# Optimization experiments

Measured on AMD Instinct MI355X. Metric: run time of the kernel, lower is better.

## Reference

```python
import jax, jax.numpy as jnp
import numpy as np

COMMITMENT_COST = 0.25


def l2norm(x, eps=1e-12):
    # F.normalize along last dim
    n = jnp.linalg.norm(x, axis=-1, keepdims=True)
    return x / jnp.maximum(n, eps)


def vector_quantize(x, codebook, commitment_cost):
    """Euclidean VQ: cdist + argmin, straight-through, VQ loss + perplexity.
    x: (B, N, D), codebook: (K, D)."""
    B, N, D = x.shape
    K = codebook.shape[0]
    flat = x.reshape(-1, D)  # (BN, D)
    # squared euclidean distances via expansion (no (BN,K,D) intermediate)
    d = (jnp.sum(flat * flat, axis=-1, keepdims=True)
         - 2.0 * flat @ codebook.T
         + jnp.sum(codebook * codebook, axis=-1))  # (BN, K)
    idx = jnp.argmin(d, axis=-1)  # (BN,)
    q = codebook[idx]  # (BN, D)
    # VQ losses
    e_latent = jnp.mean((jax.lax.stop_gradient(q) - flat) ** 2)
    q_latent = jnp.mean((q - jax.lax.stop_gradient(flat)) ** 2)
    loss = q_latent + commitment_cost * e_latent
    # perplexity over codebook usage (bincount, not dense one-hot)
    counts = jnp.zeros((K,), flat.dtype).at[idx].add(1.0)
    probs = counts / idx.shape[0]
    perplexity = jnp.exp(-jnp.sum(probs * jnp.log(probs + 1e-10)))
    return idx.reshape(B, N), perplexity, loss


def transform_mfcc(X):
    # wave_embedding.transform_freq: normalize frames, then rfft -> real -> bins 2:40
    Xn = l2norm(X)
    spec = jnp.fft.rfft(Xn, axis=-1).real[..., 2:40]  # (B, N, 38)
    return l2norm(spec)  # mfcc_embedding.norm_fn


def setup_inputs() -> dict:
    key = jax.random.key(0)
    k1, k2, k3 = jax.random.split(key, 3)
    X = jax.random.normal(k1, (16, 4096, 80), dtype=jnp.float32)
    wave_codebook = jax.random.normal(k2, (1024, 80), dtype=jnp.float32)
    mfcc_codebook = jax.random.normal(k3, (256, 38), dtype=jnp.float32)
    return {"X": X, "wave_codebook": wave_codebook, "mfcc_codebook": mfcc_codebook}


def reference(X, wave_codebook, mfcc_codebook):
    K_wave = wave_codebook.shape[0]
    wave_idx, wave_ppl, wave_loss = vector_quantize(X, wave_codebook, COMMITMENT_COST)
    X_mfcc = transform_mfcc(X)
    mfcc_idx, mfcc_ppl, mfcc_loss = vector_quantize(X_mfcc, mfcc_codebook, COMMITMENT_COST)
    mfcc_idx = mfcc_idx + K_wave
    # rearrange stack([wave, mfcc], dim=1): 'b c n -> b (n c)' -> interleave per frame
    B, N = wave_idx.shape
    encodings = jnp.stack([wave_idx, mfcc_idx], axis=-1).reshape(B, 2 * N)
    return encodings, wave_ppl, wave_loss, mfcc_ppl, mfcc_loss
```

## Files before the change

### kernel.cpp

```cpp
#include <hip/hip_runtime.h>
#include <hip/hip_bf16.h>
#include <math.h>


#define NROWS 65536
#define DW    80
#define KW    1024
#define DM    38
#define KM    256

typedef __attribute__((ext_vector_type(8))) short bf16x8;
typedef __attribute__((ext_vector_type(4))) float f32x4;

__device__ __forceinline__ void bf16split(float v, short& h, short& l) {
    __hip_bfloat16 hb = __float2bfloat16(v);
    float hf = __bfloat162float(hb);
    __hip_bfloat16 lb = __float2bfloat16(v - hf);
    h = *(short*)&hb;
    l = *(short*)&lb;
}

__device__ __forceinline__ void bf16split3(float v, short& a, short& b, short& c) {
    __hip_bfloat16 h = __float2bfloat16(v);
    float hf = __bfloat162float(h);
    float r = v - hf;
    __hip_bfloat16 m = __float2bfloat16(r);
    float mf = __bfloat162float(m);
    __hip_bfloat16 lo = __float2bfloat16(r - mf);
    a = *(short*)&h; b = *(short*)&m; c = *(short*)&lo;
}

__device__ __forceinline__ bf16x8 bf8zero() {
    bf16x8 z;
    #pragma unroll
    for (int j = 0; j < 8; ++j) z[j] = 0;
    return z;
}

__device__ __forceinline__ void wvq_tile(
    const bf16x8 (&Ah)[4][3], const bf16x8 (&Al)[4][3],
    const bf16x8 (&bh)[3], const bf16x8 (&bl)[3],
    float cnv, int idx0, float (&bd)[4][4], int (&bi)[4][4])
{
    f32x4 aL[4], aH[4];
    #pragma unroll
    for (int rt = 0; rt < 4; ++rt) {
        aL[rt] = (f32x4){0.f, 0.f, 0.f, 0.f};
        aH[rt] = (f32x4){0.f, 0.f, 0.f, 0.f};
    }
    #pragma unroll
    for (int s = 0; s < 3; ++s) {
        #pragma unroll
        for (int rt = 0; rt < 4; ++rt)
            aL[rt] = __builtin_amdgcn_mfma_f32_16x16x32_bf16(Al[rt][s], bl[s], aL[rt], 0, 0, 0);
        #pragma unroll
        for (int rt = 0; rt < 4; ++rt)
            aL[rt] = __builtin_amdgcn_mfma_f32_16x16x32_bf16(Ah[rt][s], bl[s], aL[rt], 0, 0, 0);
        #pragma unroll
        for (int rt = 0; rt < 4; ++rt)
            aH[rt] = __builtin_amdgcn_mfma_f32_16x16x32_bf16(Al[rt][s], bh[s], aH[rt], 0, 0, 0);
        #pragma unroll
        for (int rt = 0; rt < 4; ++rt)
            aH[rt] = __builtin_amdgcn_mfma_f32_16x16x32_bf16(Ah[rt][s], bh[s], aH[rt], 0, 0, 0);
    }
    #pragma unroll
    for (int rt = 0; rt < 4; ++rt)
        #pragma unroll
        for (int i = 0; i < 4; ++i) {
            float d = fmaf(-2.f, aL[rt][i] + aH[rt][i], cnv);
            if (d < bd[rt][i]) { bd[rt][i] = d; bi[rt][i] = idx0; }
        }
}

#define WS_SUMS   0
#define WS_HIST   256
#define WS_CNW    5376
#define WS_CNM    9472
#define WS_CTF    10496
#define WS_CBF    33536
#define WS_CWH    107264
#define WS_CWL    303872

__global__ __launch_bounds__(256) void prep_kernel(
    const float* __restrict__ cbw, const float* __restrict__ cbm,
    float* __restrict__ sums, int* __restrict__ hist,
    float* __restrict__ cn_w, float* __restrict__ cn_m,
    short* __restrict__ ctf, short* __restrict__ cbf,
    short* __restrict__ cwh, short* __restrict__ cwl)
{
    int idx = blockIdx.x * 256 + threadIdx.x;
    if (idx < 12288) {
        const int f = idx;
        const int ct = f / 192, rem = f % 192, s = rem >> 6, l = rem & 63;
        const int code = ct * 16 + (l & 15);
        const int k0 = 32 * s + 8 * (l >> 4);
        bf16x8 h, lo;
        if (k0 < DW) {
            const float4* p = (const float4*)(cbw + (size_t)code * DW + k0);
            float4 u = p[0], v = p[1];
            float fv[8] = {u.x, u.y, u.z, u.w, v.x, v.y, v.z, v.w};
            #pragma unroll
            for (int j = 0; j < 8; ++j) {
                short hh, ll;
                bf16split(fv[j], hh, ll);
                h[j] = hh; lo[j] = ll;
            }
        } else { h = bf8zero(); lo = bf8zero(); }
        *(bf16x8*)&cwh[(size_t)f * 8] = h;
        *(bf16x8*)&cwl[(size_t)f * 8] = lo;
    } else if (idx < 16128) {
        int t = idx - 12288;
        int col, k;
        if (t < 3072) {
            int j = t & 7, l = (t >> 3) & 63, tt = t >> 9;
            col = (tt >> 1) * 16 + (l & 15);
            k = 32 * (tt & 1) + 8 * (l >> 4) + j;
        } else {
            int i2 = t - 3072;
            int j = i2 & 7, l = (i2 >> 3) & 31, ct = i2 >> 8;
            col = ct * 16 + (l & 15);
            k = 64 + 8 * (l >> 4) + j;
        }
        float v = (col < DM)
            ? (float)cos(2.0 * 3.14159265358979323846 * (double)((col + 2) * k) / 80.0)
            : 0.f;
        short a, b, c; bf16split3(v, a, b, c);
        ctf[t] = a; ctf[3840 + t] = b; ctf[7680 + t] = c;
    } else if (idx < 28416) {
        int i3 = idx - 16128;
        int code, k;
        if (i3 < 8192) {
            int j = i3 & 7, l = (i3 >> 3) & 63, ct = i3 >> 9;
            code = ct * 16 + (l & 15);
            k = 8 * (l >> 4) + j;
        } else {
            int i4 = i3 - 8192;
            int j = i4 & 7, l = (i4 >> 3) & 31, ct = i4 >> 8;
            code = ct * 16 + (l & 15);
            k = 32 + 8 * (l >> 4) + j;
        }
        float v = (k < DM) ? cbm[(size_t)code * DM + k] : 0.f;
        short a, b, c; bf16split3(v, a, b, c);
        cbf[i3] = a; cbf[12288 + i3] = b; cbf[24576 + i3] = c;
    } else if (idx < 29440) {
        int i = idx - 28416;
        const float* p = cbw + (size_t)i * DW;
        float s = 0.f;
        for (int k = 0; k < DW; ++k) s = fmaf(p[k], p[k], s);
        cn_w[i] = s;
    } else if (idx < 29696) {
        int i = idx - 29440;
        const float* p = cbm + (size_t)i * DM;
        float s = 0.f;
        for (int j = 0; j < DM; ++j) s = fmaf(p[j], p[j], s);
        cn_m[i] = s;
    } else if (idx < 30976) {
        hist[idx - 29696] = 0;
    } else if (idx == 30976) sums[0] = 0.f;
    else if (idx == 30977)   sums[1] = 0.f;
}

__global__ __launch_bounds__(256, 2) void wave_vq_mfma(
    const float* __restrict__ X, const short* __restrict__ cwh,
    const short* __restrict__ cwl, const float* __restrict__ cn,
    float* __restrict__ out, float* __restrict__ sums)
{
    __shared__ float sd[2][64][16];
    __shared__ int   si[2][64][16];
    __shared__ float redw[2];

    const int tid  = threadIdx.x;
    const int l    = tid & 63;
    const int qu   = tid >> 6;
    const int grp  = qu >> 1;
    const int half = qu & 1;
    const int c16  = l & 15;
    const int g    = l >> 4;
    const size_t rowbase = (size_t)blockIdx.x * 128 + (size_t)grp * 64;

    bf16x8 Ah[4][3], Al[4][3];
    float xs2[4] = {0.f, 0.f, 0.f, 0.f};
    #pragma unroll
    for (int rt = 0; rt < 4; ++rt) {
        #pragma unroll
        for (int s = 0; s < 3; ++s) {
            const int k0 = 32 * s + 8 * g;
            bf16x8 ah, al;
            if (k0 < DW) {
                const float4* ap =
                    (const float4*)(X + (rowbase + rt * 16 + c16) * DW + k0);
                float4 u = ap[0], w = ap[1];
                float f[8] = {u.x, u.y, u.z, u.w, w.x, w.y, w.z, w.w};
                #pragma unroll
                for (int j = 0; j < 8; ++j) {
                    short hh, ll;
                    bf16split(f[j], hh, ll);
                    ah[j] = hh; al[j] = ll;
                    xs2[rt] = fmaf(f[j], f[j], xs2[rt]);
                }
            } else {
                ah = bf8zero(); al = bf8zero();
            }
            Ah[rt][s] = ah; Al[rt][s] = al;
        }
    }
    #pragma unroll
    for (int rt = 0; rt < 4; ++rt) {
        xs2[rt] += __shfl_xor(xs2[rt], 16, 64);
        xs2[rt] += __shfl_xor(xs2[rt], 32, 64);
    }

    float bd[4][4];
    int   bi[4][4];
    #pragma unroll
    for (int rt = 0; rt < 4; ++rt)
        #pragma unroll
        for (int i = 0; i < 4; ++i) { bd[rt][i] = 3.4e38f; bi[rt][i] = 0; }

    const bf16x8* Hp = (const bf16x8*)cwh + l;
    const bf16x8* Lp = (const bf16x8*)cwl + l;
    const int ct0 = half * 32;

    bf16x8 b0h[3], b0l[3], b1h[3], b1l[3];
    float cn0, cn1;
    #pragma unroll
    for (int s = 0; s < 3; ++s) {
        b0h[s] = Hp[(ct0 * 3 + s) * 64];
        b0l[s] = Lp[(ct0 * 3 + s) * 64];
    }
    cn0 = cn[ct0 * 16 + c16];

    #pragma unroll 1
    for (int ctl = 0; ctl < 32; ctl += 2) {
        const int ct = ct0 + ctl;
        #pragma unroll
        for (int s = 0; s < 3; ++s) {
            b1h[s] = Hp[((ct + 1) * 3 + s) * 64];
            b1l[s] = Lp[((ct + 1) * 3 + s) * 64];
        }
        cn1 = cn[(ct + 1) * 16 + c16];
        wvq_tile(Ah, Al, b0h, b0l, cn0, ct * 16 + c16, bd, bi);
        if (ctl + 2 < 32) {
            #pragma unroll
            for (int s = 0; s < 3; ++s) {
                b0h[s] = Hp[((ct + 2) * 3 + s) * 64];
                b0l[s] = Lp[((ct + 2) * 3 + s) * 64];
            }
            cn0 = cn[(ct + 2) * 16 + c16];
        }
        wvq_tile(Ah, Al, b1h, b1l, cn1, (ct + 1) * 16 + c16, bd, bi);
    }

    if (half == 1) {
        #pragma unroll
        for (int rt = 0; rt < 4; ++rt)
            #pragma unroll
            for (int i = 0; i < 4; ++i) {
                sd[grp][l][rt * 4 + i] = bd[rt][i];
                si[grp][l][rt * 4 + i] = bi[rt][i];
            }
    }
    __syncthreads();
    if (half == 0) {
        float lw = 0.f;
        #pragma unroll
        for (int rt = 0; rt < 4; ++rt) {
            #pragma unroll
            for (int i = 0; i < 4; ++i) {
                float d = bd[rt][i]; int ix = bi[rt][i];
                float dp = sd[grp][l][rt * 4 + i];
                int   ip = si[grp][l][rt * 4 + i];
                if (dp < d || (dp == d && ip < ix)) { d = dp; ix = ip; }
                #pragma unroll
                for (int m = 1; m < 16; m <<= 1) {
                    float d2 = __shfl_xor(d, m, 64);
                    int   i2 = __shfl_xor(ix, m, 64);
                    if (d2 < d || (d2 == d && i2 < ix)) { d = d2; ix = i2; }
                }
                float xn = __shfl(xs2[rt], (l & 48) + 4 * (l >> 4) + i, 64);
                if (c16 == 0) {
                    size_t row = rowbase + rt * 16 + 4 * g + i;
                    out[2 * row] = (float)ix;
                    lw += d + xn;
                }
            }
        }
        #pragma unroll
        for (int m = 1; m < 64; m <<= 1) lw += __shfl_xor(lw, m, 64);
        if (l == 0) redw[grp] = lw;
    }
    __syncthreads();
    if (tid == 0) atomicAdd(&sums[0], redw[0] + redw[1]);
}

__global__ __launch_bounds__(256, 2) void mfcc_mfma(
    const float* __restrict__ X, const float* __restrict__ cn_m,
    const short* __restrict__ ctf, const short* __restrict__ cbf,
    float* __restrict__ out, float* __restrict__ sums)
{
    __shared__ float XF[2][64 * 49];
    __shared__ float sd[2][64][16];
    __shared__ int   si[2][64][16];
    __shared__ float CN[KM];
    __shared__ float red2[2];

    const int tid  = threadIdx.x;
    const int l    = tid & 63;
    const int qu   = tid >> 6;
    const int grp  = qu >> 1;
    const int half = qu & 1;
    const int c16  = l & 15;
    const int g    = l >> 4;
    const size_t rowbase = (size_t)blockIdx.x * 128 + (size_t)grp * 64;

    CN[tid] = cn_m[tid];

    float* xfl = &XF[grp][0];

    #pragma unroll 1
    for (int rt2 = 0; rt2 < 2; ++rt2) {
        const int rt = half * 2 + rt2;
        bf16x8 A0[3], A1[3], A2[3];
        #pragma unroll
        for (int s = 0; s < 3; ++s) {
            const int k0 = 32 * s + 8 * g;
            if (k0 < DW) {
                const float4* ap =
                    (const float4*)(X + (rowbase + rt * 16 + c16) * DW + k0);
                float4 u = ap[0], v = ap[1];
                float f[8] = {u.x, u.y, u.z, u.w, v.x, v.y, v.z, v.w};
                bf16x8 a0, a1, a2;
                #pragma unroll
                for (int j = 0; j < 8; ++j) {
                    short aa, bb, cc;
                    bf16split3(f[j], aa, bb, cc);
                    a0[j] = aa; a1[j] = bb; a2[j] = cc;
                }
                A0[s] = a0; A1[s] = a1; A2[s] = a2;
            } else {
                A0[s] = bf8zero(); A1[s] = bf8zero(); A2[s] = bf8zero();
            }
        }

        f32x4 accA[3], accB[3];
        #pragma unroll
        for (int ct = 0; ct < 3; ++ct) {
            accA[ct] = (f32x4){0.f, 0.f, 0.f, 0.f};
            accB[ct] = (f32x4){0.f, 0.f, 0.f, 0.f};
        }

        #pragma unroll
        for (int s = 0; s < 3; ++s) {
            #pragma unroll
            for (int ct = 0; ct < 3; ++ct) {
                bf16x8 b0, b1, b2;
                if (s < 2) {
                    const int off = ((ct * 2 + s) * 64 + l) * 8;
                    b0 = *(const bf16x8*)&ctf[off];
                    b1 = *(const bf16x8*)&ctf[3840 + off];
                    b2 = *(const bf16x8*)&ctf[7680 + off];
                } else if (l < 32) {
                    const int off = 3072 + (ct * 32 + l) * 8;
                    b0 = *(const bf16x8*)&ctf[off];
                    b1 = *(const bf16x8*)&ctf[3840 + off];
                    b2 = *(const bf16x8*)&ctf[7680 + off];
                } else {
                    b0 = bf8zero(); b1 = bf8zero(); b2 = bf8zero();
                }
                accA[ct] = __builtin_amdgcn_mfma_f32_16x16x32_bf16(A2[s], b0, accA[ct], 0, 0, 0);
                accA[ct] = __builtin_amdgcn_mfma_f32_16x16x32_bf16(A1[s], b1, accA[ct], 0, 0, 0);
                accA[ct] = __builtin_amdgcn_mfma_f32_16x16x32_bf16(A0[s], b2, accA[ct], 0, 0, 0);
                accB[ct] = __builtin_amdgcn_mfma_f32_16x16x32_bf16(A1[s], b0, accB[ct], 0, 0, 0);
                accB[ct] = __builtin_amdgcn_mfma_f32_16x16x32_bf16(A0[s], b1, accB[ct], 0, 0, 0);
                accB[ct] = __builtin_amdgcn_mfma_f32_16x16x32_bf16(A0[s], b0, accB[ct], 0, 0, 0);
            }
        }

        f32x4 acc[3];
        #pragma unroll
        for (int ct = 0; ct < 3; ++ct) acc[ct] = accA[ct] + accB[ct];

        #pragma unroll
        for (int i = 0; i < 4; ++i) {
            float n2 = acc[0][i] * acc[0][i];
            n2 = fmaf(acc[1][i], acc[1][i], n2);
            n2 = fmaf(acc[2][i], acc[2][i], n2);
            #pragma unroll
            for (int m = 1; m < 16; m <<= 1) n2 += __shfl_xor(n2, m, 64);
            float inv = 1.0f / fmaxf(sqrtf(n2), 1e-12f);
            const int row_l = rt * 16 + 4 * g + i;
            #pragma unroll
            for (int ct = 0; ct < 3; ++ct)
                xfl[row_l * 49 + ct * 16 + c16] = acc[ct][i] * inv;
        }
    }
    __syncthreads();

    bf16x8 X0[4][3], X1[4][3];
    #pragma unroll
    for (int rt = 0; rt < 4; ++rt) {
        const int r0 = rt * 16 + c16;
        {
            const float* p = &xfl[r0 * 49 + 8 * g];
            bf16x8 q0, q1, q2;
            #pragma unroll
            for (int j = 0; j < 8; ++j) {
                short aa, bb, cc;
                bf16split3(p[j], aa, bb, cc);
                q0[j] = aa; q1[j] = bb; q2[j] = cc;
            }
            X0[rt][0] = q0; X0[rt][1] = q1; X0[rt][2] = q2;
        }
        if (g < 2) {
            const float* p = &xfl[r0 * 49 + 32 + 8 * g];
            bf16x8 q0, q1, q2;
            #pragma unroll
            for (int j = 0; j < 8; ++j) {
                short aa, bb, cc;
                bf16split3(p[j], aa, bb, cc);
                q0[j] = aa; q1[j] = bb; q2[j] = cc;
            }
            X1[rt][0] = q0; X1[rt][1] = q1; X1[rt][2] = q2;
        } else {
            X1[rt][0] = bf8zero(); X1[rt][1] = bf8zero(); X1[rt][2] = bf8zero();
        }
    }

    float bd[4][4];
    int   bi[4][4];
    #pragma unroll
    for (int rt = 0; rt < 4; ++rt)
        #pragma unroll
        for (int i = 0; i < 4; ++i) { bd[rt][i] = 3.4e38f; bi[rt][i] = 0; }

    #pragma unroll 1
    for (int ctl = 0; ctl < 8; ++ctl) {
        const int ct = half * 8 + ctl;
        bf16x8 B0[3], B1[3];
        const int off0 = (ct * 64 + l) * 8;
        B0[0] = *(const bf16x8*)&cbf[off0];
        B0[1] = *(const bf16x8*)&cbf[12288 + off0];
        B0[2] = *(const bf16x8*)&cbf[24576 + off0];
        if (l < 32) {
            const int off1 = 8192 + (ct * 32 + l) * 8;
            B1[0] = *(const bf16x8*)&cbf[off1];
            B1[1] = *(const bf16x8*)&cbf[12288 + off1];
            B1[2] = *(const bf16x8*)&cbf[24576 + off1];
        } else {
            B1[0] = bf8zero(); B1[1] = bf8zero(); B1[2] = bf8zero();
        }
        const float cnv = CN[ct * 16 + c16];
        const int idxbase = ct * 16 + c16;
        #pragma unroll
        for (int rt = 0; rt < 4; ++rt) {
            f32x4 p0 = (f32x4){0.f, 0.f, 0.f, 0.f};
            f32x4 q0 = (f32x4){0.f, 0.f, 0.f, 0.f};
            f32x4 p1 = (f32x4){0.f, 0.f, 0.f, 0.f};
            f32x4 q1 = (f32x4){0.f, 0.f, 0.f, 0.f};
            p0 = __builtin_amdgcn_mfma_f32_16x16x32_bf16(X0[rt][2], B0[0], p0, 0, 0, 0);
            p0 = __builtin_amdgcn_mfma_f32_16x16x32_bf16(X0[rt][1], B0[1], p0, 0, 0, 0);
            p0 = __builtin_amdgcn_mfma_f32_16x16x32_bf16(X0[rt][0], B0[2], p0, 0, 0, 0);
            q0 = __builtin_amdgcn_mfma_f32_16x16x32_bf16(X0[rt][1], B0[0], q0, 0, 0, 0);
            q0 = __builtin_amdgcn_mfma_f32_16x16x32_bf16(X0[rt][0], B0[1], q0, 0, 0, 0);
            q0 = __builtin_amdgcn_mfma_f32_16x16x32_bf16(X0[rt][0], B0[0], q0, 0, 0, 0);
            p1 = __builtin_amdgcn_mfma_f32_16x16x32_bf16(X1[rt][2], B1[0], p1, 0, 0, 0);
            p1 = __builtin_amdgcn_mfma_f32_16x16x32_bf16(X1[rt][1], B1[1], p1, 0, 0, 0);
            p1 = __builtin_amdgcn_mfma_f32_16x16x32_bf16(X1[rt][0], B1[2], p1, 0, 0, 0);
            q1 = __builtin_amdgcn_mfma_f32_16x16x32_bf16(X1[rt][1], B1[0], q1, 0, 0, 0);
            q1 = __builtin_amdgcn_mfma_f32_16x16x32_bf16(X1[rt][0], B1[1], q1, 0, 0, 0);
            q1 = __builtin_amdgcn_mfma_f32_16x16x32_bf16(X1[rt][0], B1[0], q1, 0, 0, 0);
            #pragma unroll
            for (int i = 0; i < 4; ++i) {
                float d = fmaf(-2.f, (p0[i] + q0[i]) + (p1[i] + q1[i]), cnv);
                if (d < bd[rt][i]) { bd[rt][i] = d; bi[rt][i] = idxbase; }
            }
        }
    }

    if (half == 1) {
        #pragma unroll
        for (int rt = 0; rt < 4; ++rt)
            #pragma unroll
            for (int i = 0; i < 4; ++i) {
                sd[grp][l][rt * 4 + i] = bd[rt][i];
                si[grp][l][rt * 4 + i] = bi[rt][i];
            }
    }
    __syncthreads();
    if (half == 0) {
        float lm = 0.f;
        #pragma unroll
        for (int rt = 0; rt < 4; ++rt) {
            #pragma unroll
            for (int i = 0; i < 4; ++i) {
                float d = bd[rt][i]; int ix = bi[rt][i];
                float dp = sd[grp][l][rt * 4 + i];
                int   ip = si[grp][l][rt * 4 + i];
                if (dp < d || (dp == d && ip < ix)) { d = dp; ix = ip; }
                #pragma unroll
                for (int m = 1; m < 16; m <<= 1) {
                    float d2 = __shfl_xor(d, m, 64);
                    int   i2 = __shfl_xor(ix, m, 64);
                    if (d2 < d || (d2 == d && i2 < ix)) { d = d2; ix = i2; }
                }
                if (c16 == 0) {
                    size_t row = rowbase + rt * 16 + 4 * g + i;
                    out[2 * row + 1] = (float)(ix + KW);
                    lm += d + 1.0f;
                }
            }
        }
        #pragma unroll
        for (int m = 1; m < 64; m <<= 1) lm += __shfl_xor(lm, m, 64);
        if (l == 0) red2[grp] = lm;
    }
    __syncthreads();
    if (tid == 0) atomicAdd(&sums[1], red2[0] + red2[1]);
}

__global__ __launch_bounds__(256) void hist_kernel(
    const float* __restrict__ out, int* __restrict__ hist)
{
    __shared__ int h[1280];
    const int tid = threadIdx.x;
    for (int i = tid; i < 1280; i += 256) h[i] = 0;
    __syncthreads();
    const int r = blockIdx.x * 256 + tid;
    float2 e = *(const float2*)&out[2 * r];
    atomicAdd(&h[(int)e.x], 1);
    atomicAdd(&h[1024 + ((int)e.y - KW)], 1);
    __syncthreads();
    for (int i = tid; i < 1280; i += 256)
        if (h[i]) atomicAdd(&hist[i], h[i]);
}

__global__ __launch_bounds__(256) void finalize_kernel(
    const int* __restrict__ hist, const float* __restrict__ sums,
    float* __restrict__ out)
{
    __shared__ float red[4];
    const int tid = threadIdx.x;
    const bool wv = (blockIdx.x == 0);
    const int K = wv ? KW : KM;
    const int base = wv ? 0 : 1024;
    float s = 0.f;
    for (int i = tid; i < K; i += 256) {
        float p = (float)hist[base + i] * (1.0f / 65536.0f);
        s += p * logf(p + 1e-10f);
    }
    #pragma unroll
    for (int off = 32; off >= 1; off >>= 1) s += __shfl_xor(s, off, 64);
    if ((tid & 63) == 0) red[tid >> 6] = s;
    __syncthreads();
    if (tid == 0) {
        float t = red[0] + red[1] + red[2] + red[3];
        float ppl = expf(-t);
        float denom = wv ? (float)(NROWS * DW) : (float)(NROWS * DM);
        int obase = 2 * NROWS + (wv ? 0 : 2);
        out[obase]     = ppl;
        out[obase + 1] = 1.25f * sums[wv ? 0 : 1] / denom;
    }
}

extern "C" void kernel_launch(void* const* d_in, const int* in_sizes, int n_in,
                              void* d_out, int out_size, void* d_ws, size_t ws_size,
                              hipStream_t stream) {
    const float* X   = (const float*)d_in[0];
    const float* cbw = (const float*)d_in[1];
    const float* cbm = (const float*)d_in[2];
    float* out = (float*)d_out;

    char* ws = (char*)d_ws;
    float* sums = (float*)(ws + WS_SUMS);
    int*   hist = (int*)(ws + WS_HIST);
    float* cn_w = (float*)(ws + WS_CNW);
    float* cn_m = (float*)(ws + WS_CNM);
    short* ctf  = (short*)(ws + WS_CTF);
    short* cbf  = (short*)(ws + WS_CBF);
    short* cwh  = (short*)(ws + WS_CWH);
    short* cwl  = (short*)(ws + WS_CWL);

    prep_kernel<<<122, 256, 0, stream>>>(cbw, cbm, sums, hist, cn_w, cn_m,
                                         ctf, cbf, cwh, cwl);
    wave_vq_mfma<<<NROWS / 128, 256, 0, stream>>>(X, cwh, cwl, cn_w, out, sums);
    mfcc_mfma<<<NROWS / 128, 256, 0, stream>>>(X, cn_m, ctf, cbf, out, sums);
    hist_kernel<<<NROWS / 256, 256, 0, stream>>>(out, hist);
    finalize_kernel<<<2, 256, 0, stream>>>(hist, sums, out);
}
```

Before: 95.28 us.

## Merge wave and MFCC VQ kernels into one launch with interleaved block roles

Replaces the separate wave and MFCC quantization kernels with a single kernel. Even blocks run the wave path and odd blocks run the MFCC path for the same 128-row tile, and shared memory is overlaid through a union. This removes one launch and the serialization gap between the two kernels, lets the two workloads overlap on the GPU, and may improve L2 reuse of X. The union sizes shared memory to the larger MFCC layout, which can lower occupancy for the wave blocks, and load balance now depends on the mix of block types.

```diff
diff --git a/kernel.cpp b/kernel.cpp
--- a/kernel.cpp
+++ b/kernel.cpp
@@ -160,14 +160,28 @@
     else if (idx == 30977)   sums[1] = 0.f;
 }
 
-__global__ __launch_bounds__(256, 2) void wave_vq_mfma(
+struct WaveSM {
+    float sd[2][64][16];
+    int   si[2][64][16];
+    float redw[2];
+};
+struct MfccSM {
+    float XF[2][64 * 49];
+    float sd[2][64][16];
+    int   si[2][64][16];
+    float CN[KM];
+    float red2[2];
+};
+union FusedSM { WaveSM w; MfccSM m; };
+
+__global__ __launch_bounds__(256, 2) void fused_vq_kernel(
     const float* __restrict__ X, const short* __restrict__ cwh,
-    const short* __restrict__ cwl, const float* __restrict__ cn,
-    float* __restrict__ out, float* __restrict__ sums)
+    const short* __restrict__ cwl, const float* __restrict__ cn_w,
+    const float* __restrict__ cn_m, const short* __restrict__ ctf,
+    const short* __restrict__ cbf, float* __restrict__ out,
+    float* __restrict__ sums)
 {
-    __shared__ float sd[2][64][16];
-    __shared__ int   si[2][64][16];
-    __shared__ float redw[2];
+    __shared__ FusedSM sm;
 
     const int tid  = threadIdx.x;
     const int l    = tid & 63;
@@ -176,346 +190,329 @@
     const int half = qu & 1;
     const int c16  = l & 15;
     const int g    = l >> 4;
-    const size_t rowbase = (size_t)blockIdx.x * 128 + (size_t)grp * 64;
-
-    bf16x8 Ah[4][3], Al[4][3];
-    float xs2[4] = {0.f, 0.f, 0.f, 0.f};
-    #pragma unroll
-    for (int rt = 0; rt < 4; ++rt) {
+    const int widx = blockIdx.x >> 1;
+    const size_t rowbase = (size_t)widx * 128 + (size_t)grp * 64;
+
+    if ((blockIdx.x & 1) == 0) {
+        bf16x8 Ah[4][3], Al[4][3];
+        float xs2[4] = {0.f, 0.f, 0.f, 0.f};
+        #pragma unroll
+        for (int rt = 0; rt < 4; ++rt) {
+            #pragma unroll
+            for (int s = 0; s < 3; ++s) {
+                const int k0 = 32 * s + 8 * g;
+                bf16x8 ah, al;
+                if (k0 < DW) {
+                    const float4* ap =
+                        (const float4*)(X + (rowbase + rt * 16 + c16) * DW + k0);
+                    float4 u = ap[0], w = ap[1];
+                    float f[8] = {u.x, u.y, u.z, u.w, w.x, w.y, w.z, w.w};
+                    #pragma unroll
+                    for (int j = 0; j < 8; ++j) {
+                        short hh, ll;
+                        bf16split(f[j], hh, ll);
+                        ah[j] = hh; al[j] = ll;
+                        xs2[rt] = fmaf(f[j], f[j], xs2[rt]);
+                    }
+                } else {
+                    ah = bf8zero(); al = bf8zero();
+                }
+                Ah[rt][s] = ah; Al[rt][s] = al;
+            }
+        }
+        #pragma unroll
+        for (int rt = 0; rt < 4; ++rt) {
+            xs2[rt] += __shfl_xor(xs2[rt], 16, 64);
+            xs2[rt] += __shfl_xor(xs2[rt], 32, 64);
+        }
+
+        float bd[4][4];
+        int   bi[4][4];
+        #pragma unroll
+        for (int rt = 0; rt < 4; ++rt)
+            #pragma unroll
+            for (int i = 0; i < 4; ++i) { bd[rt][i] = 3.4e38f; bi[rt][i] = 0; }
+
+        const bf16x8* Hp = (const bf16x8*)cwh + l;
+        const bf16x8* Lp = (const bf16x8*)cwl + l;
+        const int ct0 = half * 32;
+
+        bf16x8 b0h[3], b0l[3], b1h[3], b1l[3];
+        float cn0, cn1;
         #pragma unroll
         for (int s = 0; s < 3; ++s) {
-            const int k0 = 32 * s + 8 * g;
-            bf16x8 ah, al;
-            if (k0 < DW) {
-                const float4* ap =
-                    (const float4*)(X + (rowbase + rt * 16 + c16) * DW + k0);
-                float4 u = ap[0], w = ap[1];
-                float f[8] = {u.x, u.y, u.z, u.w, w.x, w.y, w.z, w.w};
-                #pragma unroll
-                for (int j = 0; j < 8; ++j) {
-                    short hh, ll;
-                    bf16split(f[j], hh, ll);
-                    ah[j] = hh; al[j] = ll;
-                    xs2[rt] = fmaf(f[j], f[j], xs2[rt]);
-                }
-            } else {
-                ah = bf8zero(); al = bf8zero();
-            }
-            Ah[rt][s] = ah; Al[rt][s] = al;
-        }
-    }
-    #pragma unroll
-    for (int rt = 0; rt < 4; ++rt) {
-        xs2[rt] += __shfl_xor(xs2[rt], 16, 64);
-        xs2[rt] += __shfl_xor(xs2[rt], 32, 64);
-    }
-
-    float bd[4][4];
-    int   bi[4][4];
-    #pragma unroll
-    for (int rt = 0; rt < 4; ++rt)
-        #pragma unroll
-        for (int i = 0; i < 4; ++i) { bd[rt][i] = 3.4e38f; bi[rt][i] = 0; }
-
-    const bf16x8* Hp = (const bf16x8*)cwh + l;
-    const bf16x8* Lp = (const bf16x8*)cwl + l;
-    const int ct0 = half * 32;
-
-    bf16x8 b0h[3], b0l[3], b1h[3], b1l[3];
-    float cn0, cn1;
-    #pragma unroll
-    for (int s = 0; s < 3; ++s) {
-        b0h[s] = Hp[(ct0 * 3 + s) * 64];
-        b0l[s] = Lp[(ct0 * 3 + s) * 64];
-    }
-    cn0 = cn[ct0 * 16 + c16];
-
-    #pragma unroll 1
-    for (int ctl = 0; ctl < 32; ctl += 2) {
-        const int ct = ct0 + ctl;
-        #pragma unroll
-        for (int s = 0; s < 3; ++s) {
-            b1h[s] = Hp[((ct + 1) * 3 + s) * 64];
-            b1l[s] = Lp[((ct + 1) * 3 + s) * 64];
-        }
-        cn1 = cn[(ct + 1) * 16 + c16];
-        wvq_tile(Ah, Al, b0h, b0l, cn0, ct * 16 + c16, bd, bi);
-        if (ctl + 2 < 32) {
+            b0h[s] = Hp[(ct0 * 3 + s) * 64];
+            b0l[s] = Lp[(ct0 * 3 + s) * 64];
+        }
+        cn0 = cn_w[ct0 * 16 + c16];
+
+        #pragma unroll 1
+        for (int ctl = 0; ctl < 32; ctl += 2) {
+            const int ct = ct0 + ctl;
             #pragma unroll
             for (int s = 0; s < 3; ++s) {
-                b0h[s] = Hp[((ct + 2) * 3 + s) * 64];
-                b0l[s] = Lp[((ct + 2) * 3 + s) * 64];
-            }
-            cn0 = cn[(ct + 2) * 16 + c16];
-        }
-        wvq_tile(Ah, Al, b1h, b1l, cn1, (ct + 1) * 16 + c16, bd, bi);
-    }
-
-    if (half == 1) {
-        #pragma unroll
-        for (int rt = 0; rt < 4; ++rt)
+                b1h[s] = Hp[((ct + 1) * 3 + s) * 64];
+                b1l[s] = Lp[((ct + 1) * 3 + s) * 64];
+            }
+            cn1 = cn_w[(ct + 1) * 16 + c16];
+            wvq_tile(Ah, Al, b0h, b0l, cn0, ct * 16 + c16, bd, bi);
+            if (ctl + 2 < 32) {
+                #pragma unroll
+                for (int s = 0; s < 3; ++s) {
+                    b0h[s] = Hp[((ct + 2) * 3 + s) * 64];
+                    b0l[s] = Lp[((ct + 2) * 3 + s) * 64];
+                }
+                cn0 = cn_w[(ct + 2) * 16 + c16];
+            }
+            wvq_tile(Ah, Al, b1h, b1l, cn1, (ct + 1) * 16 + c16, bd, bi);
+        }
+
+        if (half == 1) {
+            #pragma unroll
+            for (int rt = 0; rt < 4; ++rt)
+                #pragma unroll
+                for (int i = 0; i < 4; ++i) {
+                    sm.w.sd[grp][l][rt * 4 + i] = bd[rt][i];
+                    sm.w.si[grp][l][rt * 4 + i] = bi[rt][i];
+                }
+        }
+        __syncthreads();
+        if (half == 0) {
+            float lw = 0.f;
+            #pragma unroll
+            for (int rt = 0; rt < 4; ++rt) {
+                #pragma unroll
+                for (int i = 0; i < 4; ++i) {
+                    float d = bd[rt][i]; int ix = bi[rt][i];
+                    float dp = sm.w.sd[grp][l][rt * 4 + i];
+                    int   ip = sm.w.si[grp][l][rt * 4 + i];
+                    if (dp < d || (dp == d && ip < ix)) { d = dp; ix = ip; }
+                    #pragma unroll
+                    for (int m = 1; m < 16; m <<= 1) {
+                        float d2 = __shfl_xor(d, m, 64);
+                        int   i2 = __shfl_xor(ix, m, 64);
+                        if (d2 < d || (d2 == d && i2 < ix)) { d = d2; ix = i2; }
+                    }
+                    float xn = __shfl(xs2[rt], (l & 48) + 4 * (l >> 4) + i, 64);
+                    if (c16 == 0) {
+                        size_t row = rowbase + rt * 16 + 4 * g + i;
+                        out[2 * row] = (float)ix;
+                        lw += d + xn;
+                    }
+                }
+            }
+            #pragma unroll
+            for (int m = 1; m < 64; m <<= 1) lw += __shfl_xor(lw, m, 64);
+            if (l == 0) sm.w.redw[grp] = lw;
+        }
+        __syncthreads();
+        if (tid == 0) atomicAdd(&sums[0], sm.w.redw[0] + sm.w.redw[1]);
+
+    } else {
+        sm.m.CN[tid] = cn_m[tid];
+
+        float* xfl = &sm.m.XF[grp][0];
+
+        #pragma unroll 1
+        for (int rt2 = 0; rt2 < 2; ++rt2) {
+            const int rt = half * 2 + rt2;
+            bf16x8 A0[3], A1[3], A2[3];
+            #pragma unroll
+            for (int s = 0; s < 3; ++s) {
+                const int k0 = 32 * s + 8 * g;
+                if (k0 < DW) {
+                    const float4* ap =
+                        (const float4*)(X + (rowbase + rt * 16 + c16) * DW + k0);
+                    float4 u = ap[0], v = ap[1];
+                    float f[8] = {u.x, u.y, u.z, u.w, v.x, v.y, v.z, v.w};
+                    bf16x8 a0, a1, a2;
+                    #pragma unroll
+                    for (int j = 0; j < 8; ++j) {
+                        short aa, bb, cc;
+                        bf16split3(f[j], aa, bb, cc);
+                        a0[j] = aa; a1[j] = bb; a2[j] = cc;
+                    }
+                    A0[s] = a0; A1[s] = a1; A2[s] = a2;
+                } else {
+                    A0[s] = bf8zero(); A1[s] = bf8zero(); A2[s] = bf8zero();
+                }
+            }
+
+            f32x4 accA[3], accB[3];
+            #pragma unroll
+            for (int ct = 0; ct < 3; ++ct) {
+                accA[ct] = (f32x4){0.f, 0.f, 0.f, 0.f};
+                accB[ct] = (f32x4){0.f, 0.f, 0.f, 0.f};
+            }
+
+            #pragma unroll
+            for (int s = 0; s < 3; ++s) {
+                #pragma unroll
+                for (int ct = 0; ct < 3; ++ct) {
+                    bf16x8 b0, b1, b2;
+                    if (s < 2) {
+                        const int off = ((ct * 2 + s) * 64 + l) * 8;
+                        b0 = *(const bf16x8*)&ctf[off];
+                        b1 = *(const bf16x8*)&ctf[3840 + off];
+                        b2 = *(const bf16x8*)&ctf[7680 + off];
+                    } else if (l < 32) {
+                        const int off = 3072 + (ct * 32 + l) * 8;
+                        b0 = *(const bf16x8*)&ctf[off];
+                        b1 = *(const bf16x8*)&ctf[3840 + off];
+                        b2 = *(const bf16x8*)&ctf[7680 + off];
+                    } else {
+                        b0 = bf8zero(); b1 = bf8zero(); b2 = bf8zero();
+                    }
+                    accA[ct] = __builtin_amdgcn_mfma_f32_16x16x32_bf16(A2[s], b0, accA[ct], 0, 0, 0);
+                    accA[ct] = __builtin_amdgcn_mfma_f32_16x16x32_bf16(A1[s], b1, accA[ct], 0, 0, 0);
+                    accA[ct] = __builtin_amdgcn_mfma_f32_16x16x32_bf16(A0[s], b2, accA[ct], 0, 0, 0);
+                    accB[ct] = __builtin_amdgcn_mfma_f32_16x16x32_bf16(A1[s], b0, accB[ct], 0, 0, 0);
+                    accB[ct] = __builtin_amdgcn_mfma_f32_16x16x32_bf16(A0[s], b1, accB[ct], 0, 0, 0);
+                    accB[ct] = __builtin_amdgcn_mfma_f32_16x16x32_bf16(A0[s], b0, accB[ct], 0, 0, 0);
+                }
+            }
+
+            f32x4 acc[3];
+            #pragma unroll
+            for (int ct = 0; ct < 3; ++ct) acc[ct] = accA[ct] + accB[ct];
+
             #pragma unroll
             for (int i = 0; i < 4; ++i) {
-                sd[grp][l][rt * 4 + i] = bd[rt][i];
-                si[grp][l][rt * 4 + i] = bi[rt][i];
-            }
-    }
-    __syncthreads();
-    if (half == 0) {
-        float lw = 0.f;
+                float n2 = acc[0][i] * acc[0][i];
+                n2 = fmaf(acc[1][i], acc[1][i], n2);
+                n2 = fmaf(acc[2][i], acc[2][i], n2);
+                #pragma unroll
+                for (int m = 1; m < 16; m <<= 1) n2 += __shfl_xor(n2, m, 64);
+                float inv = 1.0f / fmaxf(sqrtf(n2), 1e-12f);
+                const int row_l = rt * 16 + 4 * g + i;
+                #pragma unroll
+                for (int ct = 0; ct < 3; ++ct)
+                    xfl[row_l * 49 + ct * 16 + c16] = acc[ct][i] * inv;
+            }
+        }
+        __syncthreads();
+
+        bf16x8 X0[4][3], X1[4][3];
         #pragma unroll
         for (int rt = 0; rt < 4; ++rt) {
-            #pragma unroll
-            for (int i = 0; i < 4; ++i) {
-                float d = bd[rt][i]; int ix = bi[rt][i];
-                float dp = sd[grp][l][rt * 4 + i];
-                int   ip = si[grp][l][rt * 4 + i];
-                if (dp < d || (dp == d && ip < ix)) { d = dp; ix = ip; }
-                #pragma unroll
-                for (int m = 1; m < 16; m <<= 1) {
-                    float d2 = __shfl_xor(d, m, 64);
-                    int   i2 = __shfl_xor(ix, m, 64);
-                    if (d2 < d || (d2 == d && i2 < ix)) { d = d2; ix = i2; }
-                }
-                float xn = __shfl(xs2[rt], (l & 48) + 4 * (l >> 4) + i, 64);
-                if (c16 == 0) {
-                    size_t row = rowbase + rt * 16 + 4 * g + i;
-                    out[2 * row] = (float)ix;
-                    lw += d + xn;
-                }
-            }
-        }
-        #pragma unroll
-        for (int m = 1; m < 64; m <<= 1) lw += __shfl_xor(lw, m, 64);
-        if (l == 0) redw[grp] = lw;
-    }
-    __syncthreads();
-    if (tid == 0) atomicAdd(&sums[0], redw[0] + redw[1]);
-}
-
-__global__ __launch_bounds__(256, 2) void mfcc_mfma(
-    const float* __restrict__ X, const float* __restrict__ cn_m,
-    const short* __restrict__ ctf, const short* __restrict__ cbf,
-    float* __restrict__ out, float* __restrict__ sums)
-{
-    __shared__ float XF[2][64 * 49];
-    __shared__ float sd[2][64][16];
-    __shared__ int   si[2][64][16];
-    __shared__ float CN[KM];
-    __shared__ float red2[2];
-
-    const int tid  = threadIdx.x;
-    const int l    = tid & 63;
-    const int qu   = tid >> 6;
-    const int grp  = qu >> 1;
-    const int half = qu & 1;
-    const int c16  = l & 15;
-    const int g    = l >> 4;
-    const size_t rowbase = (size_t)blockIdx.x * 128 + (size_t)grp * 64;
-
-    CN[tid] = cn_m[tid];
-
-    float* xfl = &XF[grp][0];
-
-    #pragma unroll 1
-    for (int rt2 = 0; rt2 < 2; ++rt2) {
-        const int rt = half * 2 + rt2;
-        bf16x8 A0[3], A1[3], A2[3];
-        #pragma unroll
-        for (int s = 0; s < 3; ++s) {
-            const int k0 = 32 * s + 8 * g;
-            if (k0 < DW) {
-                const float4* ap =
-                    (const float4*)(X + (rowbase + rt * 16 + c16) * DW + k0);
-                float4 u = ap[0], v = ap[1];
-                float f[8] = {u.x, u.y, u.z, u.w, v.x, v.y, v.z, v.w};
-                bf16x8 a0, a1, a2;
+            const int r0 = rt * 16 + c16;
+            {
+                const float* p = &xfl[r0 * 49 + 8 * g];
+                bf16x8 q0, q1, q2;
                 #pragma unroll
                 for (int j = 0; j < 8; ++j) {
                     short aa, bb, cc;
-                    bf16split3(f[j], aa, bb, cc);
-                    a0[j] = aa; a1[j] = bb; a2[j] = cc;
-                }
-                A0[s] = a0; A1[s] = a1; A2[s] = a2;
+                    bf16split3(p[j], aa, bb, cc);
+                    q0[j] = aa; q1[j] = bb; q2[j] = cc;
+                }
+                X0[rt][0] = q0; X0[rt][1] = q1; X0[rt][2] = q2;
+            }
+            if (g < 2) {
+                const float* p = &xfl[r0 * 49 + 32 + 8 * g];
+                bf16x8 q0, q1, q2;
+                #pragma unroll
+                for (int j = 0; j < 8; ++j) {
+                    short aa, bb, cc;
+                    bf16split3(p[j], aa, bb, cc);
+                    q0[j] = aa; q1[j] = bb; q2[j] = cc;
+                }
+                X1[rt][0] = q0; X1[rt][1] = q1; X1[rt][2] = q2;
             } else {
-                A0[s] = bf8zero(); A1[s] = bf8zero(); A2[s] = bf8zero();
-            }
-        }
-
-        f32x4 accA[3], accB[3];
-        #pragma unroll
-        for (int ct = 0; ct < 3; ++ct) {
-            accA[ct] = (f32x4){0.f, 0.f, 0.f, 0.f};
-            accB[ct] = (f32x4){0.f, 0.f, 0.f, 0.f};
-        }
-
-        #pragma unroll
-        for (int s = 0; s < 3; ++s) {
-            #pragma unroll
-            for (int ct = 0; ct < 3; ++ct) {
-                bf16x8 b0, b1, b2;
-                if (s < 2) {
-                    const int off = ((ct * 2 + s) * 64 + l) * 8;
-                    b0 = *(const bf16x8*)&ctf[off];
-                    b1 = *(const bf16x8*)&ctf[3840 + off];
-                    b2 = *(const bf16x8*)&ctf[7680 + off];
-                } else if (l < 32) {
-                    const int off = 3072 + (ct * 32 + l) * 8;
-                    b0 = *(const bf16x8*)&ctf[off];
-                    b1 = *(const bf16x8*)&ctf[3840 + off];
-                    b2 = *(const bf16x8*)&ctf[7680 + off];
-                } else {
-                    b0 = bf8zero(); b1 = bf8zero(); b2 = bf8zero();
-                }
-                accA[ct] = __builtin_amdgcn_mfma_f32_16x16x32_bf16(A2[s], b0, accA[ct], 0, 0, 0);
-                accA[ct] = __builtin_amdgcn_mfma_f32_16x16x32_bf16(A1[s], b1, accA[ct], 0, 0, 0);
-                accA[ct] = __builtin_amdgcn_mfma_f32_16x16x32_bf16(A0[s], b2, accA[ct], 0, 0, 0);
-                accB[ct] = __builtin_amdgcn_mfma_f32_16x16x32_bf16(A1[s], b0, accB[ct], 0, 0, 0);
-                accB[ct] = __builtin_amdgcn_mfma_f32_16x16x32_bf16(A0[s], b1, accB[ct], 0, 0, 0);
-                accB[ct] = __builtin_amdgcn_mfma_f32_16x16x32_bf16(A0[s], b0, accB[ct], 0, 0, 0);
-            }
-        }
-
-        f32x4 acc[3];
-        #pragma unroll
-        for (int ct = 0; ct < 3; ++ct) acc[ct] = accA[ct] + accB[ct];
-
-        #pragma unroll
-        for (int i = 0; i < 4; ++i) {
-            float n2 = acc[0][i] * acc[0][i];
-            n2 = fmaf(acc[1][i], acc[1][i], n2);
-            n2 = fmaf(acc[2][i], acc[2][i], n2);
-            #pragma unroll
-            for (int m = 1; m < 16; m <<= 1) n2 += __shfl_xor(n2, m, 64);
-            float inv = 1.0f / fmaxf(sqrtf(n2), 1e-12f);
-            const int row_l = rt * 16 + 4 * g + i;
-            #pragma unroll
-            for (int ct = 0; ct < 3; ++ct)
-                xfl[row_l * 49 + ct * 16 + c16] = acc[ct][i] * inv;
-        }
+                X1[rt][0] = bf8zero(); X1[rt][1] = bf8zero(); X1[rt][2] = bf8zero();
+            }
+        }
+
+        float bd[4][4];
+        int   bi[4][4];
+        #pragma unroll
+        for (int rt = 0; rt < 4; ++rt)
+            #pragma unroll
+            for (int i = 0; i < 4; ++i) { bd[rt][i] = 3.4e38f; bi[rt][i] = 0; }
+
+        #pragma unroll 1
+        for (int ctl = 0; ctl < 8; ++ctl) {
+            const int ct = half * 8 + ctl;
+            bf16x8 B0[3], B1[3];
+            const int off0 = (ct * 64 + l) * 8;
+            B0[0] = *(const bf16x8*)&cbf[off0];
+            B0[1] = *(const bf16x8*)&cbf[12288 + off0];
+            B0[2] = *(const bf16x8*)&cbf[24576 + off0];
+            if (l < 32) {
+                const int off1 = 8192 + (ct * 32 + l) * 8;
+                B1[0] = *(const bf16x8*)&cbf[off1];
+                B1[1] = *(const bf16x8*)&cbf[12288 + off1];
+                B1[2] = *(const bf16x8*)&cbf[24576 + off1];
+            } else {
+                B1[0] = bf8zero(); B1[1] = bf8zero(); B1[2] = bf8zero();
+            }
+            const float cnv = sm.m.CN[ct * 16 + c16];
+            const int idxbase = ct * 16 + c16;
+            #pragma unroll
+            for (int rt = 0; rt < 4; ++rt) {
+                f32x4 p0 = (f32x4){0.f, 0.f, 0.f, 0.f};
+                f32x4 q0 = (f32x4){0.f, 0.f, 0.f, 0.f};
+                f32x4 p1 = (f32x4){0.f, 0.f, 0.f, 0.f};
+                f32x4 q1 = (f32x4){0.f, 0.f, 0.f, 0.f};
+                p0 = __builtin_amdgcn_mfma_f32_16x16x32_bf16(X0[rt][2], B0[0], p0, 0, 0, 0);
+                p0 = __builtin_amdgcn_mfma_f32_16x16x32_bf16(X0[rt][1], B0[1], p0, 0, 0, 0);
+                p0 = __builtin_amdgcn_mfma_f32_16x16x32_bf16(X0[rt][0], B0[2], p0, 0, 0, 0);
+                q0 = __builtin_amdgcn_mfma_f32_16x16x32_bf16(X0[rt][1], B0[0], q0, 0, 0, 0);
+                q0 = __builtin_amdgcn_mfma_f32_16x16x32_bf16(X0[rt][0], B0[1], q0, 0, 0, 0);
+                q0 = __builtin_amdgcn_mfma_f32_16x16x32_bf16(X0[rt][0], B0[0], q0, 0, 0, 0);
+                p1 = __builtin_amdgcn_mfma_f32_16x16x32_bf16(X1[rt][2], B1[0], p1, 0, 0, 0);
+                p1 = __builtin_amdgcn_mfma_f32_16x16x32_bf16(X1[rt][1], B1[1], p1, 0, 0, 0);
+                p1 = __builtin_amdgcn_mfma_f32_16x16x32_bf16(X1[rt][0], B1[2], p1, 0, 0, 0);
+                q1 = __builtin_amdgcn_mfma_f32_16x16x32_bf16(X1[rt][1], B1[0], q1, 0, 0, 0);
+                q1 = __builtin_amdgcn_mfma_f32_16x16x32_bf16(X1[rt][0], B1[1], q1, 0, 0, 0);
+                q1 = __builtin_amdgcn_mfma_f32_16x16x32_bf16(X1[rt][0], B1[0], q1, 0, 0, 0);
+                #pragma unroll
+                for (int i = 0; i < 4; ++i) {
+                    float d = fmaf(-2.f, (p0[i] + q0[i]) + (p1[i] + q1[i]), cnv);
+                    if (d < bd[rt][i]) { bd[rt][i] = d; bi[rt][i] = idxbase; }
+                }
+            }
+        }
+
+        if (half == 1) {
+            #pragma unroll
+            for (int rt = 0; rt < 4; ++rt)
+                #pragma unroll
+                for (int i = 0; i < 4; ++i) {
+                    sm.m.sd[grp][l][rt * 4 + i] = bd[rt][i];
+                    sm.m.si[grp][l][rt * 4 + i] = bi[rt][i];
+                }
+        }
+        __syncthreads();
+        if (half == 0) {
+            float lm = 0.f;
+            #pragma unroll
+            for (int rt = 0; rt < 4; ++rt) {
+                #pragma unroll
+                for (int i = 0; i < 4; ++i) {
+                    float d = bd[rt][i]; int ix = bi[rt][i];
+                    float dp = sm.m.sd[grp][l][rt * 4 + i];
+                    int   ip = sm.m.si[grp][l][rt * 4 + i];
+                    if (dp < d || (dp == d && ip < ix)) { d = dp; ix = ip; }
+                    #pragma unroll
+                    for (int m = 1; m < 16; m <<= 1) {
+                        float d2 = __shfl_xor(d, m, 64);
+                        int   i2 = __shfl_xor(ix, m, 64);
+                        if (d2 < d || (d2 == d && i2 < ix)) { d = d2; ix = i2; }
+                    }
+                    if (c16 == 0) {
+                        size_t row = rowbase + rt * 16 + 4 * g + i;
+                        out[2 * row + 1] = (float)(ix + KW);
+                        lm += d + 1.0f;
+                    }
+                }
+            }
+            #pragma unroll
+            for (int m = 1; m < 64; m <<= 1) lm += __shfl_xor(lm, m, 64);
+            if (l == 0) sm.m.red2[grp] = lm;
+        }
+        __syncthreads();
+        if (tid == 0) atomicAdd(&sums[1], sm.m.red2[0] + sm.m.red2[1]);
     }
-    __syncthreads();
-
-    bf16x8 X0[4][3], X1[4][3];
-    #pragma unroll
-    for (int rt = 0; rt < 4; ++rt) {
-        const int r0 = rt * 16 + c16;
-        {
-            const float* p = &xfl[r0 * 49 + 8 * g];
-            bf16x8 q0, q1, q2;
-            #pragma unroll
-            for (int j = 0; j < 8; ++j) {
-                short aa, bb, cc;
-                bf16split3(p[j], aa, bb, cc);
-                q0[j] = aa; q1[j] = bb; q2[j] = cc;
-            }
-            X0[rt][0] = q0; X0[rt][1] = q1; X0[rt][2] = q2;
-        }
-        if (g < 2) {
-            const float* p = &xfl[r0 * 49 + 32 + 8 * g];
-            bf16x8 q0, q1, q2;
-            #pragma unroll
-            for (int j = 0; j < 8; ++j) {
-                short aa, bb, cc;
-                bf16split3(p[j], aa, bb, cc);
-                q0[j] = aa; q1[j] = bb; q2[j] = cc;
-            }
-            X1[rt][0] = q0; X1[rt][1] = q1; X1[rt][2] = q2;
-        } else {
-            X1[rt][0] = bf8zero(); X1[rt][1] = bf8zero(); X1[rt][2] = bf8zero();
-        }
-    }
-
-    float bd[4][4];
-    int   bi[4][4];
-    #pragma unroll
-    for (int rt = 0; rt < 4; ++rt)
-        #pragma unroll
-        for (int i = 0; i < 4; ++i) { bd[rt][i] = 3.4e38f; bi[rt][i] = 0; }
-
-    #pragma unroll 1
-    for (int ctl = 0; ctl < 8; ++ctl) {
-        const int ct = half * 8 + ctl;
-        bf16x8 B0[3], B1[3];
-        const int off0 = (ct * 64 + l) * 8;
-        B0[0] = *(const bf16x8*)&cbf[off0];
-        B0[1] = *(const bf16x8*)&cbf[12288 + off0];
-        B0[2] = *(const bf16x8*)&cbf[24576 + off0];
-        if (l < 32) {
-            const int off1 = 8192 + (ct * 32 + l) * 8;
-            B1[0] = *(const bf16x8*)&cbf[off1];
-            B1[1] = *(const bf16x8*)&cbf[12288 + off1];
-            B1[2] = *(const bf16x8*)&cbf[24576 + off1];
-        } else {
-            B1[0] = bf8zero(); B1[1] = bf8zero(); B1[2] = bf8zero();
-        }
-        const float cnv = CN[ct * 16 + c16];
-        const int idxbase = ct * 16 + c16;
-        #pragma unroll
-        for (int rt = 0; rt < 4; ++rt) {
-            f32x4 p0 = (f32x4){0.f, 0.f, 0.f, 0.f};
-            f32x4 q0 = (f32x4){0.f, 0.f, 0.f, 0.f};
-            f32x4 p1 = (f32x4){0.f, 0.f, 0.f, 0.f};
-            f32x4 q1 = (f32x4){0.f, 0.f, 0.f, 0.f};
-            p0 = __builtin_amdgcn_mfma_f32_16x16x32_bf16(X0[rt][2], B0[0], p0, 0, 0, 0);
-            p0 = __builtin_amdgcn_mfma_f32_16x16x32_bf16(X0[rt][1], B0[1], p0, 0, 0, 0);
-            p0 = __builtin_amdgcn_mfma_f32_16x16x32_bf16(X0[rt][0], B0[2], p0, 0, 0, 0);
-            q0 = __builtin_amdgcn_mfma_f32_16x16x32_bf16(X0[rt][1], B0[0], q0, 0, 0, 0);
-            q0 = __builtin_amdgcn_mfma_f32_16x16x32_bf16(X0[rt][0], B0[1], q0, 0, 0, 0);
-            q0 = __builtin_amdgcn_mfma_f32_16x16x32_bf16(X0[rt][0], B0[0], q0, 0, 0, 0);
-            p1 = __builtin_amdgcn_mfma_f32_16x16x32_bf16(X1[rt][2], B1[0], p1, 0, 0, 0);
-            p1 = __builtin_amdgcn_mfma_f32_16x16x32_bf16(X1[rt][1], B1[1], p1, 0, 0, 0);
-            p1 = __builtin_amdgcn_mfma_f32_16x16x32_bf16(X1[rt][0], B1[2], p1, 0, 0, 0);
-            q1 = __builtin_amdgcn_mfma_f32_16x16x32_bf16(X1[rt][1], B1[0], q1, 0, 0, 0);
-            q1 = __builtin_amdgcn_mfma_f32_16x16x32_bf16(X1[rt][0], B1[1], q1, 0, 0, 0);
-            q1 = __builtin_amdgcn_mfma_f32_16x16x32_bf16(X1[rt][0], B1[0], q1, 0, 0, 0);
-            #pragma unroll
-            for (int i = 0; i < 4; ++i) {
-                float d = fmaf(-2.f, (p0[i] + q0[i]) + (p1[i] + q1[i]), cnv);
-                if (d < bd[rt][i]) { bd[rt][i] = d; bi[rt][i] = idxbase; }
-            }
-        }
-    }
-
-    if (half == 1) {
-        #pragma unroll
-        for (int rt = 0; rt < 4; ++rt)
-            #pragma unroll
-            for (int i = 0; i < 4; ++i) {
-                sd[grp][l][rt * 4 + i] = bd[rt][i];
-                si[grp][l][rt * 4 + i] = bi[rt][i];
-            }
-    }
-    __syncthreads();
-    if (half == 0) {
-        float lm = 0.f;
-        #pragma unroll
-        for (int rt = 0; rt < 4; ++rt) {
-            #pragma unroll
-            for (int i = 0; i < 4; ++i) {
-                float d = bd[rt][i]; int ix = bi[rt][i];
-                float dp = sd[grp][l][rt * 4 + i];
-                int   ip = si[grp][l][rt * 4 + i];
-                if (dp < d || (dp == d && ip < ix)) { d = dp; ix = ip; }
-                #pragma unroll
-                for (int m = 1; m < 16; m <<= 1) {
-                    float d2 = __shfl_xor(d, m, 64);
-                    int   i2 = __shfl_xor(ix, m, 64);
-                    if (d2 < d || (d2 == d && i2 < ix)) { d = d2; ix = i2; }
-                }
-                if (c16 == 0) {
-                    size_t row = rowbase + rt * 16 + 4 * g + i;
-                    out[2 * row + 1] = (float)(ix + KW);
-                    lm += d + 1.0f;
-                }
-            }
-        }
-        #pragma unroll
-        for (int m = 1; m < 64; m <<= 1) lm += __shfl_xor(lm, m, 64);
-        if (l == 0) red2[grp] = lm;
-    }
-    __syncthreads();
-    if (tid == 0) atomicAdd(&sums[1], red2[0] + red2[1]);
 }
 
 __global__ __launch_bounds__(256) void hist_kernel(
@@ -582,8 +579,8 @@
 
     prep_kernel<<<122, 256, 0, stream>>>(cbw, cbm, sums, hist, cn_w, cn_m,
                                          ctf, cbf, cwh, cwl);
-    wave_vq_mfma<<<NROWS / 128, 256, 0, stream>>>(X, cwh, cwl, cn_w, out, sums);
-    mfcc_mfma<<<NROWS / 128, 256, 0, stream>>>(X, cn_m, ctf, cbf, out, sums);
+    fused_vq_kernel<<<NROWS / 64, 256, 0, stream>>>(X, cwh, cwl, cn_w, cn_m,
+                                                    ctf, cbf, out, sums);
     hist_kernel<<<NROWS / 256, 256, 0, stream>>>(out, hist);
     finalize_kernel<<<2, 256, 0, stream>>>(hist, sums, out);
 }
```

Measured after the change: 99.83 us. 1.05x slower.
